# Performance work log

Hardware: AMD Instinct MI355X
Metric: run time of the kernel (lower is better)

The kernel has to match this reference:

```python
import jax, jax.numpy as jnp
import numpy as np

NEG = -10000.0
EPS = 1e-5

B, N, H, DEPTH = 4096, 64, 128, 3
H2 = H // 2


def setup_inputs() -> dict:
    key = jax.random.key(0)
    k1, k2, k3 = jax.random.split(key, 3)
    hidden_states = jax.random.normal(k1, (B, N, H), dtype=jnp.float32)
    li_vector_num = jax.random.randint(k2, (B,), 0, N + 1, dtype=jnp.int32)
    Ws = jax.random.normal(k3, (DEPTH, H, H2), dtype=jnp.float32) * (1.0 / np.sqrt(H))
    bs = jnp.zeros((DEPTH, H2), dtype=jnp.float32)
    ln_w = jnp.ones((DEPTH, H2), dtype=jnp.float32)
    ln_b = jnp.zeros((DEPTH, H2), dtype=jnp.float32)
    return {"hidden_states": hidden_states, "li_vector_num": li_vector_num,
            "Ws": Ws, "bs": bs, "ln_w": ln_w, "ln_b": ln_b}


def _subgraph(hidden_states, Ws, bs, ln_w, ln_b, li_vector_num):
    b, n, h = hidden_states.shape
    # padding mask: -10000 for invalid vectors (i >= li_vector_num), per polyline
    pad = jnp.where(jnp.arange(n)[None, :] >= li_vector_num[:, None], NEG, 0.0)
    pad = pad.astype(hidden_states.dtype)[:, :, None]  # [B,N,1]
    hs = hidden_states
    for l in range(Ws.shape[0]):
        # MLP: linear -> layernorm -> relu
        x = jnp.einsum('bnh,hk->bnk', hs, Ws[l]) + bs[l]
        mu = jnp.mean(x, axis=-1, keepdims=True)
        var = jnp.mean((x - mu) ** 2, axis=-1, keepdims=True)
        x = ln_w[l] * (x - mu) * jax.lax.rsqrt(var + EPS) + ln_b[l]
        enc = jax.nn.relu(x)  # [B,N,H2]
        m = enc + pad  # masked encoded states
        # leave-one-out max over vector dim via top-2 trick (replaces O(N^2) loop)
        top2 = jax.lax.top_k(jnp.swapaxes(m, 1, 2), 2)[0]  # [B,H2,2]
        top1b = top2[..., 0][:, None, :]  # [B,1,H2]
        top2b = top2[..., 1][:, None, :]  # [B,1,H2]
        loo = jnp.where(m == top1b, top2b, top1b)  # max over i != j
        loo = jnp.maximum(loo, m + NEG)            # faithful: j itself at -10000
        loo = jnp.maximum(loo, 0.0)                # torch.max(max_hidden, zeros)
        hs = jnp.concatenate([enc, loo], axis=-1)  # [B,N,H]
    return jnp.max(hs, axis=1)  # [B,H]


def reference(hidden_states, li_vector_num, Ws, bs, ln_w, ln_b):
    return _subgraph(hidden_states, Ws, bs, ln_w, ln_b, li_vector_num)
```

## Files before the change

kernel.cpp:

```cpp
#include <hip/hip_runtime.h>
#include <hip/hip_bf16.h>

#define NEGV (-10000.0f)
#define EPSV (1e-5f)
#define NINF (-3.4e38f)

typedef __attribute__((ext_vector_type(8))) short short8;
typedef __attribute__((ext_vector_type(4))) float floatx4;

constexpr int Bsz = 4096, Nv = 64, Hd = 128, DEPTH = 3, H2 = 64;
constexpr int ESTR = 72;

struct alignas(8) BH4 { __hip_bfloat162 a, b; };

__device__ __forceinline__ unsigned short f2b(float f) {
    unsigned int u = __builtin_bit_cast(unsigned int, f);
    u += 0x7fffu + ((u >> 16) & 1u);
    return (unsigned short)(u >> 16);
}

template <int CTRL>
__device__ __forceinline__ float dpp_add(float v) {
    int y = __builtin_amdgcn_update_dpp(0, __builtin_bit_cast(int, v), CTRL, 0xf, 0xf, true);
    return v + __builtin_bit_cast(float, y);
}
__device__ __forceinline__ float sum16(float v) {
    v = dpp_add<0xB1>(v);
    v = dpp_add<0x4E>(v);
    v = dpp_add<0x124>(v);
    v = dpp_add<0x128>(v);
    return v;
}

__device__ __forceinline__ void t2insIdx(float& t1, float& t2, unsigned& i1,
                                         float v, unsigned iv) {
    bool c = v > t1;
    float lo = fminf(t1, v);
    t1 = fmaxf(t1, v);
    i1 = c ? iv : i1;
    t2 = fmaxf(t2, lo);
}

__global__ void prep_w(const float* __restrict__ Ws, unsigned short* __restrict__ wt) {
    int idx = blockIdx.x * 256 + threadIdx.x;
    if (idx < DEPTH * 8192) {
        int l = idx >> 13, o = idx & 8191;
        int j = o & 7, q = (o >> 3) & 63, hi = (o >> 9) & 3, kt = o >> 11;
        int k = kt * 32 + hi * 8 + j;
        int srccol = (q & 15) * 4 + (q >> 4);
        wt[idx] = f2b(Ws[l * 8192 + k * 64 + srccol]);
    }
}

__global__
void subgraph_kernel(const float* __restrict__ hidden, const int* __restrict__ lvn,
                     const unsigned short* __restrict__ wt,
                     const float* __restrict__ bsv, const float* __restrict__ lnw,
                     const float* __restrict__ lnb, float* __restrict__ out)
{
    __shared__ __hip_bfloat16 encs[4][16][ESTR];
    __shared__ float fbuf3[4][4][3][64];
    __shared__ float apk[64][2];
    __shared__ unsigned short aidx[64];

    const int t = threadIdx.x;
    const int lane = t & 63, wid = t >> 6;
    const int b = blockIdx.x;
    const int lr = lane & 15, hi = lane >> 4;
    const int L = lvn[b];
    const unsigned myrow = wid * 16 + lr;

    float madd[4];
#pragma unroll
    for (int reg = 0; reg < 4; ++reg)
        madd[reg] = ((int)(wid * 16 + hi * 4 + reg) >= L) ? NEGV : 0.0f;

    const float4* ab = (const float4*)(hidden + (size_t)b * Nv * Hd);

#pragma unroll
    for (int l = 0; l < DEPTH; ++l) {
        const short8* wfrag = (const short8*)(wt + l * 8192);

        short8 af[4];
        if (l == 0) {
#pragma unroll
            for (int kt = 0; kt < 4; ++kt) {
                int fi = (int)myrow * 32 + kt * 8 + hi * 2;
                float4 f0 = ab[fi], f1 = ab[fi + 1];
                union { short8 s; __hip_bfloat162 h[4]; } u;
                u.h[0] = __float22bfloat162_rn(make_float2(f0.x, f0.y));
                u.h[1] = __float22bfloat162_rn(make_float2(f0.z, f0.w));
                u.h[2] = __float22bfloat162_rn(make_float2(f1.x, f1.y));
                u.h[3] = __float22bfloat162_rn(make_float2(f1.z, f1.w));
                af[kt] = u.s;
            }
        } else {
            af[0] = *(const short8*)&encs[wid][lr][hi * 8];
            af[1] = *(const short8*)&encs[wid][lr][32 + hi * 8];
#pragma unroll
            for (int kt = 2; kt < 4; ++kt) {
                int cbase = (kt - 2) * 32 + hi * 8;
                short8 ar = *(const short8*)&aidx[cbase];
                const float4* ap = (const float4*)&apk[0][0];
                int fb = cbase >> 1;
                float4 q0 = ap[fb], q1 = ap[fb + 1], q2 = ap[fb + 2], q3 = ap[fb + 3];
                unsigned pk1s[8] = {
                    __builtin_bit_cast(unsigned, q0.x), __builtin_bit_cast(unsigned, q0.z),
                    __builtin_bit_cast(unsigned, q1.x), __builtin_bit_cast(unsigned, q1.z),
                    __builtin_bit_cast(unsigned, q2.x), __builtin_bit_cast(unsigned, q2.z),
                    __builtin_bit_cast(unsigned, q3.x), __builtin_bit_cast(unsigned, q3.z)};
                unsigned pk2s[8] = {
                    __builtin_bit_cast(unsigned, q0.y), __builtin_bit_cast(unsigned, q0.w),
                    __builtin_bit_cast(unsigned, q1.y), __builtin_bit_cast(unsigned, q1.w),
                    __builtin_bit_cast(unsigned, q2.y), __builtin_bit_cast(unsigned, q2.w),
                    __builtin_bit_cast(unsigned, q3.y), __builtin_bit_cast(unsigned, q3.w)};
                union { short8 s; unsigned u[4]; } uu;
#pragma unroll
                for (int j2 = 0; j2 < 4; ++j2) {
                    unsigned s0 = ((unsigned)(unsigned short)ar[2 * j2]     == myrow)
                                  ? pk2s[2 * j2]     : pk1s[2 * j2];
                    unsigned s1 = ((unsigned)(unsigned short)ar[2 * j2 + 1] == myrow)
                                  ? pk2s[2 * j2 + 1] : pk1s[2 * j2 + 1];
                    uu.u[j2] = __builtin_amdgcn_perm(s1, s0, 0x05040100u);
                }
                af[kt] = uu.s;
            }
        }

        floatx4 acc[4];
#pragma unroll
        for (int ct = 0; ct < 4; ++ct) { floatx4 z = {0.f, 0.f, 0.f, 0.f}; acc[ct] = z; }
#pragma unroll
        for (int kt = 0; kt < 4; ++kt)
#pragma unroll
            for (int ct = 0; ct < 4; ++ct) {
                short8 bf = wfrag[(kt * 4 + hi) * 64 + ct * 16 + lr];
                acc[ct] = __builtin_amdgcn_mfma_f32_16x16x32_bf16(af[kt], bf, acc[ct], 0, 0, 0);
            }

        float4 bias = *(const float4*)(bsv + l * H2 + 4 * lr);
        float4 gwv  = *(const float4*)(lnw + l * H2 + 4 * lr);
        float4 gbv  = *(const float4*)(lnb + l * H2 + 4 * lr);
#pragma unroll
        for (int reg = 0; reg < 4; ++reg) {
            float x0 = acc[0][reg] + bias.x;
            float x1 = acc[1][reg] + bias.y;
            float x2 = acc[2][reg] + bias.z;
            float x3 = acc[3][reg] + bias.w;
            float s = sum16((x0 + x1) + (x2 + x3));
            float q = sum16((x0 * x0 + x1 * x1) + (x2 * x2 + x3 * x3));
            float mu  = s * (1.0f / 64.0f);
            float var = fmaxf(q * (1.0f / 64.0f) - mu * mu, 0.0f);
            float rstd = rsqrtf(var + EPSV);
            acc[0][reg] = fmaxf(gwv.x * (x0 - mu) * rstd + gbv.x, 0.0f);
            acc[1][reg] = fmaxf(gwv.y * (x1 - mu) * rstd + gbv.y, 0.0f);
            acc[2][reg] = fmaxf(gwv.z * (x2 - mu) * rstd + gbv.z, 0.0f);
            acc[3][reg] = fmaxf(gwv.w * (x3 - mu) * rstd + gbv.w, 0.0f);
        }

        if (l < DEPTH - 1) {
            float t1v[4] = {NINF, NINF, NINF, NINF}, t2v[4] = {NINF, NINF, NINF, NINF};
            unsigned i1v[4] = {0, 0, 0, 0};
#pragma unroll
            for (int reg = 0; reg < 4; ++reg) {
                BH4 we;
                we.a = __float22bfloat162_rn(make_float2(acc[0][reg], acc[1][reg]));
                we.b = __float22bfloat162_rn(make_float2(acc[2][reg], acc[3][reg]));
                *(BH4*)&encs[wid][hi * 4 + reg][4 * lr] = we;
                float mk = madd[reg];
                unsigned rowi = wid * 16 + hi * 4 + reg;
                t2insIdx(t1v[0], t2v[0], i1v[0], acc[0][reg] + mk, rowi);
                t2insIdx(t1v[1], t2v[1], i1v[1], acc[1][reg] + mk, rowi);
                t2insIdx(t1v[2], t2v[2], i1v[2], acc[2][reg] + mk, rowi);
                t2insIdx(t1v[3], t2v[3], i1v[3], acc[3][reg] + mk, rowi);
            }
            *(float4*)&fbuf3[wid][hi][0][4 * lr] = make_float4(t1v[0], t1v[1], t1v[2], t1v[3]);
            *(float4*)&fbuf3[wid][hi][1][4 * lr] = make_float4(t2v[0], t2v[1], t2v[2], t2v[3]);
            *(float4*)&fbuf3[wid][hi][2][4 * lr] = make_float4(
                __builtin_bit_cast(float, i1v[0]), __builtin_bit_cast(float, i1v[1]),
                __builtin_bit_cast(float, i1v[2]), __builtin_bit_cast(float, i1v[3]));
            __syncthreads();

            if (t < 64) {
                int c = t;
                float m1 = NINF, m2 = NINF; unsigned a1 = 0;
#pragma unroll
                for (int w = 0; w < 4; ++w)
#pragma unroll
                    for (int h = 0; h < 4; ++h) {
                        float o1 = fbuf3[w][h][0][c], o2 = fbuf3[w][h][1][c];
                        unsigned io = __builtin_bit_cast(unsigned, fbuf3[w][h][2][c]);
                        bool cg = o1 > m1;
                        float lo = fminf(m1, o1);
                        m1 = fmaxf(m1, o1);
                        a1 = cg ? io : a1;
                        m2 = fmaxf(fmaxf(m2, o2), lo);
                    }
                float F1 = fmaxf(m1, 0.0f), F2 = fmaxf(m2, 0.0f);
                apk[c][0] = __builtin_bit_cast(float, (unsigned)f2b(F1));
                apk[c][1] = __builtin_bit_cast(float, (unsigned)f2b(F2));
                aidx[c] = (unsigned short)a1;
            }
            __syncthreads();
        } else {
            float t1v[4], em4[4];
#pragma unroll
            for (int ct = 0; ct < 4; ++ct) {
                float a = acc[ct][0], b2 = acc[ct][1];
                float c2 = acc[ct][2], d = acc[ct][3];
                em4[ct] = fmaxf(fmaxf(a, b2), fmaxf(c2, d));
                t1v[ct] = fmaxf(fmaxf(a + madd[0], b2 + madd[1]),
                                fmaxf(c2 + madd[2], d + madd[3]));
            }
            *(float4*)&fbuf3[wid][hi][0][4 * lr] = make_float4(t1v[0], t1v[1], t1v[2], t1v[3]);
            *(float4*)&fbuf3[wid][hi][1][4 * lr] = make_float4(em4[0], em4[1], em4[2], em4[3]);
            __syncthreads();

            if (t < 64) {
                int c = t;
                float mm = NINF, me = NINF;
#pragma unroll
                for (int w = 0; w < 4; ++w)
#pragma unroll
                    for (int h = 0; h < 4; ++h) {
                        mm = fmaxf(mm, fbuf3[w][h][0][c]);
                        me = fmaxf(me, fbuf3[w][h][1][c]);
                    }
                out[(size_t)b * Hd + c]      = me;
                out[(size_t)b * Hd + 64 + c] = fmaxf(mm, 0.0f);
            }
        }
    }
}

extern "C" void kernel_launch(void* const* d_in, const int* in_sizes, int n_in,
                              void* d_out, int out_size, void* d_ws, size_t ws_size,
                              hipStream_t stream) {
    const float* hidden = (const float*)d_in[0];
    const int*   lvn    = (const int*)d_in[1];
    const float* Ws     = (const float*)d_in[2];
    const float* bs     = (const float*)d_in[3];
    const float* lnwp   = (const float*)d_in[4];
    const float* lnbp   = (const float*)d_in[5];
    unsigned short* wt  = (unsigned short*)d_ws;
    float* outp = (float*)d_out;

    prep_w<<<(DEPTH * 8192 + 255) / 256, 256, 0, stream>>>(Ws, wt);
    subgraph_kernel<<<Bsz, 256, 0, stream>>>(hidden, lvn, wt, bs, lnwp, lnbp, outp);
}
```

Baseline: 63.43 us.

## Process two 16-row tiles per wave with 128-thread blocks, pack argmax into float

Each block now runs two waves instead of four, and each wave computes two 16-row MFMA tiles, so every weight fragment loaded from global memory feeds two MFMAs. The cross-wave top-2 reduction buffer shrinks because the argmax row index is packed into the low 6 mantissa bits of the top-1 value, which removes the third index plane. The goal is fewer weight loads per row, less shared memory and a cheaper reduction. In exchange each wave holds twice the accumulators and fragments, which raises register pressure. The packing also slightly perturbs the top-1 values used for comparison.

```diff
diff --git a/kernel.cpp b/kernel.cpp
--- a/kernel.cpp
+++ b/kernel.cpp
@@ -58,22 +58,24 @@
                      const float* __restrict__ bsv, const float* __restrict__ lnw,
                      const float* __restrict__ lnb, float* __restrict__ out)
 {
-    __shared__ __hip_bfloat16 encs[4][16][ESTR];
-    __shared__ float fbuf3[4][4][3][64];
+    __shared__ __hip_bfloat16 encs[64][ESTR];
+    __shared__ float fb[2][4][2][64];
     __shared__ float apk[64][2];
     __shared__ unsigned short aidx[64];
 
     const int t = threadIdx.x;
-    const int lane = t & 63, wid = t >> 6;
+    const int lane = t & 63, w = t >> 6;
     const int b = blockIdx.x;
     const int lr = lane & 15, hi = lane >> 4;
     const int L = lvn[b];
-    const unsigned myrow = wid * 16 + lr;
-
-    float madd[4];
-#pragma unroll
-    for (int reg = 0; reg < 4; ++reg)
-        madd[reg] = ((int)(wid * 16 + hi * 4 + reg) >= L) ? NEGV : 0.0f;
+    const unsigned myrow[2] = {(unsigned)(w * 32 + lr), (unsigned)(w * 32 + 16 + lr)};
+
+    float madd[2][4];
+#pragma unroll
+    for (int rt = 0; rt < 2; ++rt)
+#pragma unroll
+        for (int reg = 0; reg < 4; ++reg)
+            madd[rt][reg] = ((w * 32 + rt * 16 + hi * 4 + reg) >= L) ? NEGV : 0.0f;
 
     const float4* ab = (const float4*)(hidden + (size_t)b * Nv * Hd);
 
@@ -81,29 +83,34 @@
     for (int l = 0; l < DEPTH; ++l) {
         const short8* wfrag = (const short8*)(wt + l * 8192);
 
-        short8 af[4];
+        short8 af[2][4];
         if (l == 0) {
 #pragma unroll
-            for (int kt = 0; kt < 4; ++kt) {
-                int fi = (int)myrow * 32 + kt * 8 + hi * 2;
-                float4 f0 = ab[fi], f1 = ab[fi + 1];
-                union { short8 s; __hip_bfloat162 h[4]; } u;
-                u.h[0] = __float22bfloat162_rn(make_float2(f0.x, f0.y));
-                u.h[1] = __float22bfloat162_rn(make_float2(f0.z, f0.w));
-                u.h[2] = __float22bfloat162_rn(make_float2(f1.x, f1.y));
-                u.h[3] = __float22bfloat162_rn(make_float2(f1.z, f1.w));
-                af[kt] = u.s;
-            }
+            for (int rt = 0; rt < 2; ++rt)
+#pragma unroll
+                for (int kt = 0; kt < 4; ++kt) {
+                    int fi = (int)myrow[rt] * 32 + kt * 8 + hi * 2;
+                    float4 f0 = ab[fi], f1 = ab[fi + 1];
+                    union { short8 s; __hip_bfloat162 h[4]; } u;
+                    u.h[0] = __float22bfloat162_rn(make_float2(f0.x, f0.y));
+                    u.h[1] = __float22bfloat162_rn(make_float2(f0.z, f0.w));
+                    u.h[2] = __float22bfloat162_rn(make_float2(f1.x, f1.y));
+                    u.h[3] = __float22bfloat162_rn(make_float2(f1.z, f1.w));
+                    af[rt][kt] = u.s;
+                }
         } else {
-            af[0] = *(const short8*)&encs[wid][lr][hi * 8];
-            af[1] = *(const short8*)&encs[wid][lr][32 + hi * 8];
+#pragma unroll
+            for (int rt = 0; rt < 2; ++rt) {
+                af[rt][0] = *(const short8*)&encs[myrow[rt]][hi * 8];
+                af[rt][1] = *(const short8*)&encs[myrow[rt]][32 + hi * 8];
+            }
 #pragma unroll
             for (int kt = 2; kt < 4; ++kt) {
                 int cbase = (kt - 2) * 32 + hi * 8;
                 short8 ar = *(const short8*)&aidx[cbase];
                 const float4* ap = (const float4*)&apk[0][0];
-                int fb = cbase >> 1;
-                float4 q0 = ap[fb], q1 = ap[fb + 1], q2 = ap[fb + 2], q3 = ap[fb + 3];
+                int fbq = cbase >> 1;
+                float4 q0 = ap[fbq], q1 = ap[fbq + 1], q2 = ap[fbq + 2], q3 = ap[fbq + 3];
                 unsigned pk1s[8] = {
                     __builtin_bit_cast(unsigned, q0.x), __builtin_bit_cast(unsigned, q0.z),
                     __builtin_bit_cast(unsigned, q1.x), __builtin_bit_cast(unsigned, q1.z),
@@ -114,91 +121,103 @@
                     __builtin_bit_cast(unsigned, q1.y), __builtin_bit_cast(unsigned, q1.w),
                     __builtin_bit_cast(unsigned, q2.y), __builtin_bit_cast(unsigned, q2.w),
                     __builtin_bit_cast(unsigned, q3.y), __builtin_bit_cast(unsigned, q3.w)};
-                union { short8 s; unsigned u[4]; } uu;
-#pragma unroll
-                for (int j2 = 0; j2 < 4; ++j2) {
-                    unsigned s0 = ((unsigned)(unsigned short)ar[2 * j2]     == myrow)
-                                  ? pk2s[2 * j2]     : pk1s[2 * j2];
-                    unsigned s1 = ((unsigned)(unsigned short)ar[2 * j2 + 1] == myrow)
-                                  ? pk2s[2 * j2 + 1] : pk1s[2 * j2 + 1];
-                    uu.u[j2] = __builtin_amdgcn_perm(s1, s0, 0x05040100u);
+#pragma unroll
+                for (int rt = 0; rt < 2; ++rt) {
+                    union { short8 s; unsigned u[4]; } uu;
+#pragma unroll
+                    for (int j2 = 0; j2 < 4; ++j2) {
+                        unsigned s0 = ((unsigned)(unsigned short)ar[2 * j2]     == myrow[rt])
+                                      ? pk2s[2 * j2]     : pk1s[2 * j2];
+                        unsigned s1 = ((unsigned)(unsigned short)ar[2 * j2 + 1] == myrow[rt])
+                                      ? pk2s[2 * j2 + 1] : pk1s[2 * j2 + 1];
+                        uu.u[j2] = __builtin_amdgcn_perm(s1, s0, 0x05040100u);
+                    }
+                    af[rt][kt] = uu.s;
                 }
-                af[kt] = uu.s;
             }
         }
 
-        floatx4 acc[4];
-#pragma unroll
-        for (int ct = 0; ct < 4; ++ct) { floatx4 z = {0.f, 0.f, 0.f, 0.f}; acc[ct] = z; }
+        floatx4 acc[2][4];
+#pragma unroll
+        for (int rt = 0; rt < 2; ++rt)
+#pragma unroll
+            for (int ct = 0; ct < 4; ++ct) { floatx4 z = {0.f, 0.f, 0.f, 0.f}; acc[rt][ct] = z; }
 #pragma unroll
         for (int kt = 0; kt < 4; ++kt)
 #pragma unroll
             for (int ct = 0; ct < 4; ++ct) {
                 short8 bf = wfrag[(kt * 4 + hi) * 64 + ct * 16 + lr];
-                acc[ct] = __builtin_amdgcn_mfma_f32_16x16x32_bf16(af[kt], bf, acc[ct], 0, 0, 0);
+                acc[0][ct] = __builtin_amdgcn_mfma_f32_16x16x32_bf16(af[0][kt], bf, acc[0][ct], 0, 0, 0);
+                acc[1][ct] = __builtin_amdgcn_mfma_f32_16x16x32_bf16(af[1][kt], bf, acc[1][ct], 0, 0, 0);
             }
 
         float4 bias = *(const float4*)(bsv + l * H2 + 4 * lr);
         float4 gwv  = *(const float4*)(lnw + l * H2 + 4 * lr);
         float4 gbv  = *(const float4*)(lnb + l * H2 + 4 * lr);
 #pragma unroll
-        for (int reg = 0; reg < 4; ++reg) {
-            float x0 = acc[0][reg] + bias.x;
-            float x1 = acc[1][reg] + bias.y;
-            float x2 = acc[2][reg] + bias.z;
-            float x3 = acc[3][reg] + bias.w;
-            float s = sum16((x0 + x1) + (x2 + x3));
-            float q = sum16((x0 * x0 + x1 * x1) + (x2 * x2 + x3 * x3));
-            float mu  = s * (1.0f / 64.0f);
-            float var = fmaxf(q * (1.0f / 64.0f) - mu * mu, 0.0f);
-            float rstd = rsqrtf(var + EPSV);
-            acc[0][reg] = fmaxf(gwv.x * (x0 - mu) * rstd + gbv.x, 0.0f);
-            acc[1][reg] = fmaxf(gwv.y * (x1 - mu) * rstd + gbv.y, 0.0f);
-            acc[2][reg] = fmaxf(gwv.z * (x2 - mu) * rstd + gbv.z, 0.0f);
-            acc[3][reg] = fmaxf(gwv.w * (x3 - mu) * rstd + gbv.w, 0.0f);
-        }
+        for (int rt = 0; rt < 2; ++rt)
+#pragma unroll
+            for (int reg = 0; reg < 4; ++reg) {
+                float x0 = acc[rt][0][reg] + bias.x;
+                float x1 = acc[rt][1][reg] + bias.y;
+                float x2 = acc[rt][2][reg] + bias.z;
+                float x3 = acc[rt][3][reg] + bias.w;
+                float s = sum16((x0 + x1) + (x2 + x3));
+                float q = sum16((x0 * x0 + x1 * x1) + (x2 * x2 + x3 * x3));
+                float mu  = s * (1.0f / 64.0f);
+                float var = fmaxf(q * (1.0f / 64.0f) - mu * mu, 0.0f);
+                float rstd = rsqrtf(var + EPSV);
+                acc[rt][0][reg] = fmaxf(gwv.x * (x0 - mu) * rstd + gbv.x, 0.0f);
+                acc[rt][1][reg] = fmaxf(gwv.y * (x1 - mu) * rstd + gbv.y, 0.0f);
+                acc[rt][2][reg] = fmaxf(gwv.z * (x2 - mu) * rstd + gbv.z, 0.0f);
+                acc[rt][3][reg] = fmaxf(gwv.w * (x3 - mu) * rstd + gbv.w, 0.0f);
+            }
 
         if (l < DEPTH - 1) {
             float t1v[4] = {NINF, NINF, NINF, NINF}, t2v[4] = {NINF, NINF, NINF, NINF};
             unsigned i1v[4] = {0, 0, 0, 0};
 #pragma unroll
-            for (int reg = 0; reg < 4; ++reg) {
-                BH4 we;
-                we.a = __float22bfloat162_rn(make_float2(acc[0][reg], acc[1][reg]));
-                we.b = __float22bfloat162_rn(make_float2(acc[2][reg], acc[3][reg]));
-                *(BH4*)&encs[wid][hi * 4 + reg][4 * lr] = we;
-                float mk = madd[reg];
-                unsigned rowi = wid * 16 + hi * 4 + reg;
-                t2insIdx(t1v[0], t2v[0], i1v[0], acc[0][reg] + mk, rowi);
-                t2insIdx(t1v[1], t2v[1], i1v[1], acc[1][reg] + mk, rowi);
-                t2insIdx(t1v[2], t2v[2], i1v[2], acc[2][reg] + mk, rowi);
-                t2insIdx(t1v[3], t2v[3], i1v[3], acc[3][reg] + mk, rowi);
-            }
-            *(float4*)&fbuf3[wid][hi][0][4 * lr] = make_float4(t1v[0], t1v[1], t1v[2], t1v[3]);
-            *(float4*)&fbuf3[wid][hi][1][4 * lr] = make_float4(t2v[0], t2v[1], t2v[2], t2v[3]);
-            *(float4*)&fbuf3[wid][hi][2][4 * lr] = make_float4(
-                __builtin_bit_cast(float, i1v[0]), __builtin_bit_cast(float, i1v[1]),
-                __builtin_bit_cast(float, i1v[2]), __builtin_bit_cast(float, i1v[3]));
+            for (int rt = 0; rt < 2; ++rt)
+#pragma unroll
+                for (int reg = 0; reg < 4; ++reg) {
+                    BH4 we;
+                    we.a = __float22bfloat162_rn(make_float2(acc[rt][0][reg], acc[rt][1][reg]));
+                    we.b = __float22bfloat162_rn(make_float2(acc[rt][2][reg], acc[rt][3][reg]));
+                    *(BH4*)&encs[w * 32 + rt * 16 + hi * 4 + reg][4 * lr] = we;
+                    float mk = madd[rt][reg];
+                    unsigned rowi = w * 32 + rt * 16 + hi * 4 + reg;
+                    t2insIdx(t1v[0], t2v[0], i1v[0], acc[rt][0][reg] + mk, rowi);
+                    t2insIdx(t1v[1], t2v[1], i1v[1], acc[rt][1][reg] + mk, rowi);
+                    t2insIdx(t1v[2], t2v[2], i1v[2], acc[rt][2][reg] + mk, rowi);
+                    t2insIdx(t1v[3], t2v[3], i1v[3], acc[rt][3][reg] + mk, rowi);
+                }
+            float4 w0, w1;
+#pragma unroll
+            for (int ct = 0; ct < 4; ++ct) {
+                unsigned bits = (__builtin_bit_cast(unsigned, t1v[ct]) & ~63u) | i1v[ct];
+                (&w0.x)[ct] = __builtin_bit_cast(float, bits);
+                (&w1.x)[ct] = t2v[ct];
+            }
+            *(float4*)&fb[w][hi][0][4 * lr] = w0;
+            *(float4*)&fb[w][hi][1][4 * lr] = w1;
             __syncthreads();
 
             if (t < 64) {
                 int c = t;
                 float m1 = NINF, m2 = NINF; unsigned a1 = 0;
 #pragma unroll
-                for (int w = 0; w < 4; ++w)
+                for (int ww = 0; ww < 2; ++ww)
 #pragma unroll
                     for (int h = 0; h < 4; ++h) {
-                        float o1 = fbuf3[w][h][0][c], o2 = fbuf3[w][h][1][c];
-                        unsigned io = __builtin_bit_cast(unsigned, fbuf3[w][h][2][c]);
+                        float o1 = fb[ww][h][0][c], o2 = fb[ww][h][1][c];
                         bool cg = o1 > m1;
                         float lo = fminf(m1, o1);
                         m1 = fmaxf(m1, o1);
-                        a1 = cg ? io : a1;
+                        a1 = cg ? (__builtin_bit_cast(unsigned, o1) & 63u) : a1;
                         m2 = fmaxf(fmaxf(m2, o2), lo);
                     }
-                float F1 = fmaxf(m1, 0.0f), F2 = fmaxf(m2, 0.0f);
-                apk[c][0] = __builtin_bit_cast(float, (unsigned)f2b(F1));
-                apk[c][1] = __builtin_bit_cast(float, (unsigned)f2b(F2));
+                apk[c][0] = __builtin_bit_cast(float, (unsigned)f2b(fmaxf(m1, 0.0f)));
+                apk[c][1] = __builtin_bit_cast(float, (unsigned)f2b(fmaxf(m2, 0.0f)));
                 aidx[c] = (unsigned short)a1;
             }
             __syncthreads();
@@ -206,25 +225,31 @@
             float t1v[4], em4[4];
 #pragma unroll
             for (int ct = 0; ct < 4; ++ct) {
-                float a = acc[ct][0], b2 = acc[ct][1];
-                float c2 = acc[ct][2], d = acc[ct][3];
-                em4[ct] = fmaxf(fmaxf(a, b2), fmaxf(c2, d));
-                t1v[ct] = fmaxf(fmaxf(a + madd[0], b2 + madd[1]),
-                                fmaxf(c2 + madd[2], d + madd[3]));
-            }
-            *(float4*)&fbuf3[wid][hi][0][4 * lr] = make_float4(t1v[0], t1v[1], t1v[2], t1v[3]);
-            *(float4*)&fbuf3[wid][hi][1][4 * lr] = make_float4(em4[0], em4[1], em4[2], em4[3]);
+                float a0 = acc[0][ct][0], a1_ = acc[0][ct][1];
+                float a2 = acc[0][ct][2], a3 = acc[0][ct][3];
+                float b0 = acc[1][ct][0], b1 = acc[1][ct][1];
+                float b2 = acc[1][ct][2], b3 = acc[1][ct][3];
+                em4[ct] = fmaxf(fmaxf(fmaxf(a0, a1_), fmaxf(a2, a3)),
+                                fmaxf(fmaxf(b0, b1), fmaxf(b2, b3)));
+                t1v[ct] = fmaxf(
+                    fmaxf(fmaxf(a0 + madd[0][0], a1_ + madd[0][1]),
+                          fmaxf(a2 + madd[0][2], a3 + madd[0][3])),
+                    fmaxf(fmaxf(b0 + madd[1][0], b1 + madd[1][1]),
+                          fmaxf(b2 + madd[1][2], b3 + madd[1][3])));
+            }
+            *(float4*)&fb[w][hi][0][4 * lr] = make_float4(t1v[0], t1v[1], t1v[2], t1v[3]);
+            *(float4*)&fb[w][hi][1][4 * lr] = make_float4(em4[0], em4[1], em4[2], em4[3]);
             __syncthreads();
 
             if (t < 64) {
                 int c = t;
                 float mm = NINF, me = NINF;
 #pragma unroll
-                for (int w = 0; w < 4; ++w)
+                for (int ww = 0; ww < 2; ++ww)
 #pragma unroll
                     for (int h = 0; h < 4; ++h) {
-                        mm = fmaxf(mm, fbuf3[w][h][0][c]);
-                        me = fmaxf(me, fbuf3[w][h][1][c]);
+                        mm = fmaxf(mm, fb[ww][h][0][c]);
+                        me = fmaxf(me, fb[ww][h][1][c]);
                     }
                 out[(size_t)b * Hd + c]      = me;
                 out[(size_t)b * Hd + 64 + c] = fmaxf(mm, 0.0f);
@@ -246,5 +271,5 @@
     float* outp = (float*)d_out;
 
     prep_w<<<(DEPTH * 8192 + 255) / 256, 256, 0, stream>>>(Ws, wt);
-    subgraph_kernel<<<Bsz, 256, 0, stream>>>(hidden, lvn, wt, bs, lnwp, lnbp, outp);
-}
+    subgraph_kernel<<<Bsz, 128, 0, stream>>>(hidden, lvn, wt, bs, lnwp, lnbp, outp);
+}
```

Result: slower. 67.44 us (+6.3%).
